# Optimization experiments

Hardware: AMD Instinct MI355X
Metric: run time of the kernel (lower is better)

## Reference

```python
import jax, jax.numpy as jnp
import numpy as np

N, E, C, R, B = 16384, 262144, 256, 9, 4


def _basis_mm(x, coeff, basis):
    # x: [E, Cin], coeff = att[edge_type]: [E, B], basis: [B, Cin, Cout]
    # equals x_e @ (sum_b coeff[e,b] * basis_b) = x_e @ W[edge_type[e]]
    h = jnp.einsum('ec,bco->ebo', x, basis)          # [E, B, Cout]
    return jnp.einsum('ebo,eb->eo', h, coeff)        # [E, Cout]


def _segment_softmax(score, gkey, nseg):
    smax = jax.ops.segment_max(score, gkey, num_segments=nseg)
    ex = jnp.exp(score - smax[gkey])
    den = jax.ops.segment_sum(ex, gkey, num_segments=nseg)
    return ex / den[gkey]


def _attn_branch(rel_emb, basis, att, aw, ab, etypes, seg):
    # relation-specific transform of edge features -> node messages
    m = _basis_mm(rel_emb, att[etypes], basis)                       # [E, Cn]
    # per-relation Linear (weight aw[r], bias ab[r]) + leaky_relu (slope 0.01)
    score = jax.nn.leaky_relu(jnp.sum(m * aw[etypes], -1) + ab[etypes])
    # original: softmax over dest index with -1e8 on edges of other relations,
    # then zeroed by mask == softmax within (dest node, relation) groups
    alpha = _segment_softmax(score, seg * R + etypes, N * R)         # [E]
    agg = jax.ops.segment_sum(alpha[:, None] * m, seg, num_segments=N)  # [N, Cn]
    onehot = jax.nn.one_hot(etypes, R, dtype=m.dtype)
    cnt = jax.ops.segment_sum(onehot, seg, num_segments=N)           # [N, R]
    div = (cnt > 0).astype(m.dtype).sum(-1)
    div = jnp.where(div == 0, jnp.ones_like(div), div)
    return agg / div[:, None]


def setup_inputs():
    key = jax.random.key(0)
    ks = jax.random.split(key, 16)
    p = lambda k, shp: jax.random.normal(k, shp, jnp.float32) * 0.05
    return {
        'edge_index': jax.random.randint(ks[0], (2, E), 0, N, dtype=jnp.int32),
        'nf': jax.random.normal(ks[1], (N, C), jnp.float32),
        'ef': jax.random.normal(ks[2], (E, C), jnp.float32),
        'edge_type_rel': jax.random.randint(ks[3], (E,), 0, R, dtype=jnp.int32),
        'edge_type_rel_inv': jax.random.randint(ks[4], (E,), 0, R, dtype=jnp.int32),
        'edge_norm': jax.random.uniform(ks[5], (E,), jnp.float32),
        'sub2rel_basis': p(ks[6], (B, C, C)),
        'sub2rel_att': p(ks[7], (R, B)),
        'obj2rel_basis': p(ks[8], (B, C, C)),
        'obj2rel_att': p(ks[9], (R, B)),
        'rel2sub_basis': p(ks[10], (B, C, C)),
        'rel2sub_att': p(ks[11], (R, B)),
        'rel2sub_attn_w': p(ks[12], (R, C)),
        'rel2sub_attn_b': jnp.zeros((R,), jnp.float32),
        'rel2obj_basis': p(ks[13], (B, C, C)),
        'rel2obj_att': p(ks[14], (R, B)),
        'rel2obj_attn_w': p(ks[15], (R, C)),
        'rel2obj_attn_b': jnp.zeros((R,), jnp.float32),
    }


def reference(edge_index, nf, ef, edge_type_rel, edge_type_rel_inv, edge_norm,
              sub2rel_basis, sub2rel_att, obj2rel_basis, obj2rel_att,
              rel2sub_basis, rel2sub_att, rel2sub_attn_w, rel2sub_attn_b,
              rel2obj_basis, rel2obj_att, rel2obj_attn_w, rel2obj_attn_b):
    src, dst = edge_index[0], edge_index[1]
    # sub2rel / obj2rel: per-edge relation-specific GEMM (mask+sum over rel in
    # the original collapses to a gather of W by edge type)
    s2r = _basis_mm(nf[src], sub2rel_att[edge_type_rel], sub2rel_basis)
    o2r = _basis_mm(nf[dst], obj2rel_att[edge_type_rel_inv], obj2rel_basis)
    rel_emb = ef + 0.5 * (s2r + o2r)
    # rel2sub aggregates at src (edgeindex_i = edge_index[0], rel types = inv)
    sub_agg = _attn_branch(rel_emb, rel2sub_basis, rel2sub_att,
                           rel2sub_attn_w, rel2sub_attn_b, edge_type_rel_inv, src)
    # rel2obj aggregates at dst (edgeindex_i = edge_index[1], rel types = fwd)
    obj_agg = _attn_branch(rel_emb, rel2obj_basis, rel2obj_att,
                           rel2obj_attn_w, rel2obj_attn_b, edge_type_rel, dst)
    node_emb = nf + 0.5 * (sub_agg + obj_agg)
    return node_emb, rel_emb
```

## Files before the change

### kernel.cpp

```cpp
#include <hip/hip_runtime.h>

#define N_ 16384
#define E_ 262144
#define C_ 256
#define R_ 9
#define B_ 4
#define NKEY (N_ * R_)
#define NKEY2 (2 * NKEY)

typedef unsigned short u16;
typedef unsigned int u32;

typedef __bf16 bf16x8 __attribute__((ext_vector_type(8)));
typedef float f32x4 __attribute__((ext_vector_type(4)));
typedef unsigned short u16x8 __attribute__((ext_vector_type(8)));

__device__ __forceinline__ u16 f2bf(float x) {
  u32 u = __float_as_uint(x);
  u32 r = (u + 0x7fffu + ((u >> 16) & 1u)) >> 16;
  return (u16)r;
}
__device__ __forceinline__ float bf2f(u16 h) {
  return __uint_as_float(((u32)h) << 16);
}

__device__ __forceinline__ void gld16(const void* g, void* l) {
  __builtin_amdgcn_global_load_lds(
      (const __attribute__((address_space(1))) void*)g,
      (__attribute__((address_space(3))) void*)l, 16, 0, 0);
}

__global__ __launch_bounds__(256) void prep_kernel(
    const float* __restrict__ b1, const float* __restrict__ a1,
    const float* __restrict__ b2, const float* __restrict__ a2,
    const float* __restrict__ b3, const float* __restrict__ a3,
    const float* __restrict__ aw3,
    const float* __restrict__ b4, const float* __restrict__ a4,
    const float* __restrict__ aw4,
    u16* __restrict__ W1, u16* __restrict__ W2,
    u16* __restrict__ W3, u16* __restrict__ W4,
    float* __restrict__ v3, float* __restrict__ v4) {
  int c = blockIdx.x, r = blockIdx.y, o = threadIdx.x;
  float s1 = 0.f, s2 = 0.f, s3 = 0.f, s4 = 0.f;
#pragma unroll
  for (int b = 0; b < B_; ++b) {
    long bi = ((long)b * C_ + c) * C_ + o;
    s1 += a1[r * B_ + b] * b1[bi];
    s2 += a2[r * B_ + b] * b2[bi];
    s3 += a3[r * B_ + b] * b3[bi];
    s4 += a4[r * B_ + b] * b4[bi];
  }
  W1[((long)r * C_ + o) * C_ + c] = f2bf(s1);
  W2[((long)r * C_ + o) * C_ + c] = f2bf(s2);
  W3[(long)o * (R_ * C_) + r * C_ + c] = f2bf(s3);
  W4[(long)o * (R_ * C_) + r * C_ + c] = f2bf(s4);

  __shared__ float red[256];
  red[o] = s3 * aw3[r * C_ + o];
  __syncthreads();
  for (int s = 128; s > 0; s >>= 1) {
    if (o < s) red[o] += red[o + s];
    __syncthreads();
  }
  float rv3 = red[0];
  __syncthreads();
  red[o] = s4 * aw4[r * C_ + o];
  __syncthreads();
  for (int s = 128; s > 0; s >>= 1) {
    if (o < s) red[o] += red[o + s];
    __syncthreads();
  }
  if (o == 0) {
    v3[r * C_ + c] = rv3;
    v4[r * C_ + c] = red[0];
  }
}

__global__ void cvt_bf16_kernel(const float* __restrict__ in, u16* __restrict__ out) {
  long i = ((long)blockIdx.x * 256 + threadIdx.x) * 4;
  float4 f = *(const float4*)(in + i);
  ushort4 h;
  h.x = f2bf(f.x); h.y = f2bf(f.y); h.z = f2bf(f.z); h.w = f2bf(f.w);
  *(ushort4*)(out + i) = h;
}

#define BM 128
#define BN 128
#define BK 32

__global__ __launch_bounds__(256) void gemmY_kernel(
    const u16* __restrict__ A, int lda,
    const u16* __restrict__ Bt0, const u16* __restrict__ Bt1, long bBatch, int K,
    u16* __restrict__ Out0, u16* __restrict__ Out1, long cBatch, int ldc) {
  __shared__ __attribute__((aligned(16))) u16 As[BM * BK];
  __shared__ __attribute__((aligned(16))) u16 Bs[BN * BK];

  const int t = threadIdx.x;
  const int m0 = blockIdx.x * BM;
  const int n0 = blockIdx.y * BN;
  const int zb = blockIdx.z;
  const long z = (zb < R_) ? zb : zb - R_;
  const u16* Bt = (zb < R_) ? Bt0 : Bt1;
  u16* Out = (zb < R_) ? Out0 : Out1;

  const int sr = t >> 2;
  const int sk = (t & 3) * 8;

  const int w = t >> 6, lane = t & 63;
  const int wm = (w >> 1) * 64, wn = (w & 1) * 64;
  const int lr = lane & 15;
  const int lk = (lane >> 4) * 8;

  f32x4 acc[4][4];
#pragma unroll
  for (int i = 0; i < 4; ++i)
#pragma unroll
    for (int j = 0; j < 4; ++j) acc[i][j] = (f32x4){0.f, 0.f, 0.f, 0.f};

  const u16* aR = A + (long)(m0 + sr) * lda + sk;
  const u16* bR = Bt + z * bBatch + (long)(n0 + sr) * K + sk;
  const long aStep = 64L * lda;
  const long bStep = 64L * K;

  u16* aD0 = &As[t * 8];
  u16* aD1 = &As[2048 + t * 8];
  u16* bD0 = &Bs[t * 8];
  u16* bD1 = &Bs[2048 + t * 8];

  for (int k0 = 0; k0 < K; k0 += BK) {
    gld16(aR, aD0);
    gld16(aR + aStep, aD1);
    gld16(bR, bD0);
    gld16(bR + bStep, bD1);
    aR += BK;
    bR += BK;
    __syncthreads();

    bf16x8 af[4], bg[4];
#pragma unroll
    for (int mi = 0; mi < 4; ++mi)
      af[mi] = *(const bf16x8*)&As[(wm + mi * 16 + lr) * BK + lk];
#pragma unroll
    for (int ni = 0; ni < 4; ++ni)
      bg[ni] = *(const bf16x8*)&Bs[(wn + ni * 16 + lr) * BK + lk];
#pragma unroll
    for (int mi = 0; mi < 4; ++mi)
#pragma unroll
      for (int ni = 0; ni < 4; ++ni)
        acc[mi][ni] = __builtin_amdgcn_mfma_f32_16x16x32_bf16(af[mi], bg[ni], acc[mi][ni], 0, 0, 0);

    __syncthreads();
  }

  long base = z * cBatch;
#pragma unroll
  for (int mi = 0; mi < 4; ++mi) {
    int rowb = m0 + wm + mi * 16 + ((lane >> 4) * 4);
#pragma unroll
    for (int ni = 0; ni < 4; ++ni) {
      int col = n0 + wn + ni * 16 + lr;
      f32x4 c = acc[mi][ni];
#pragma unroll
      for (int i = 0; i < 4; ++i) {
        long idx = base + (long)(rowb + i) * ldc + col;
        Out[idx] = f2bf(c[i]);
      }
    }
  }
}

__global__ __launch_bounds__(256) void gemmAgg_kernel(
    const u16* __restrict__ AS, const u16* __restrict__ AO,
    const u16* __restrict__ BtS, const u16* __restrict__ BtO,
    float* __restrict__ Out,
    const float* __restrict__ nf,
    const float* __restrict__ divS, const float* __restrict__ divO) {
  const int K = R_ * C_;
  __shared__ __attribute__((aligned(16))) u16 As[64 * BK];
  __shared__ __attribute__((aligned(16))) u16 Bs[BN * BK];

  const int t = threadIdx.x;
  const int m0 = blockIdx.x * 64;
  const int n0 = blockIdx.y * BN;

  const int sr = t >> 2;
  const int sk = (t & 3) * 8;

  const int w = t >> 6, lane = t & 63;
  const int wm = (w >> 1) * 32, wn = (w & 1) * 64;
  const int lr = lane & 15;
  const int lk = (lane >> 4) * 8;

  u16* aD = &As[t * 8];
  u16* bD0 = &Bs[t * 8];
  u16* bD1 = &Bs[2048 + t * 8];
  const long bStep = 64L * K;

  f32x4 accS[2][4], accO[2][4];
#pragma unroll
  for (int i = 0; i < 2; ++i)
#pragma unroll
    for (int j = 0; j < 4; ++j) {
      accS[i][j] = (f32x4){0.f, 0.f, 0.f, 0.f};
      accO[i][j] = (f32x4){0.f, 0.f, 0.f, 0.f};
    }

  {
    const u16* aR = AS + (long)(m0 + sr) * K + sk;
    const u16* bR = BtS + (long)(n0 + sr) * K + sk;
    for (int k0 = 0; k0 < K; k0 += BK) {
      gld16(aR, aD);
      gld16(bR, bD0);
      gld16(bR + bStep, bD1);
      aR += BK;
      bR += BK;
      __syncthreads();
      bf16x8 af[2], bg[4];
#pragma unroll
      for (int mi = 0; mi < 2; ++mi)
        af[mi] = *(const bf16x8*)&As[(wm + mi * 16 + lr) * BK + lk];
#pragma unroll
      for (int ni = 0; ni < 4; ++ni)
        bg[ni] = *(const bf16x8*)&Bs[(wn + ni * 16 + lr) * BK + lk];
#pragma unroll
      for (int mi = 0; mi < 2; ++mi)
#pragma unroll
        for (int ni = 0; ni < 4; ++ni)
          accS[mi][ni] = __builtin_amdgcn_mfma_f32_16x16x32_bf16(af[mi], bg[ni], accS[mi][ni], 0, 0, 0);
      __syncthreads();
    }
  }
  {
    const u16* aR = AO + (long)(m0 + sr) * K + sk;
    const u16* bR = BtO + (long)(n0 + sr) * K + sk;
    for (int k0 = 0; k0 < K; k0 += BK) {
      gld16(aR, aD);
      gld16(bR, bD0);
      gld16(bR + bStep, bD1);
      aR += BK;
      bR += BK;
      __syncthreads();
      bf16x8 af[2], bg[4];
#pragma unroll
      for (int mi = 0; mi < 2; ++mi)
        af[mi] = *(const bf16x8*)&As[(wm + mi * 16 + lr) * BK + lk];
#pragma unroll
      for (int ni = 0; ni < 4; ++ni)
        bg[ni] = *(const bf16x8*)&Bs[(wn + ni * 16 + lr) * BK + lk];
#pragma unroll
      for (int mi = 0; mi < 2; ++mi)
#pragma unroll
        for (int ni = 0; ni < 4; ++ni)
          accO[mi][ni] = __builtin_amdgcn_mfma_f32_16x16x32_bf16(af[mi], bg[ni], accO[mi][ni], 0, 0, 0);
      __syncthreads();
    }
  }

#pragma unroll
  for (int mi = 0; mi < 2; ++mi) {
    int rowb = m0 + wm + mi * 16 + ((lane >> 4) * 4);
    float fsS[4], fsO[4];
#pragma unroll
    for (int i = 0; i < 4; ++i) {
      fsS[i] = 0.5f * divS[rowb + i];
      fsO[i] = 0.5f * divO[rowb + i];
    }
#pragma unroll
    for (int ni = 0; ni < 4; ++ni) {
      int col = n0 + wn + ni * 16 + lr;
      f32x4 cS = accS[mi][ni];
      f32x4 cO = accO[mi][ni];
#pragma unroll
      for (int i = 0; i < 4; ++i) {
        long idx = (long)(rowb + i) * C_ + col;
        Out[idx] = nf[idx] + fsS[i] * cS[i] + fsO[i] * cO[i];
      }
    }
  }
}

__global__ __launch_bounds__(256) void relemb_kernel(
    const float* __restrict__ ef, const u16* __restrict__ Ysub,
    const u16* __restrict__ Yobj, const int* __restrict__ src,
    const int* __restrict__ dst, const int* __restrict__ et,
    const int* __restrict__ eti, const float* __restrict__ vS,
    const float* __restrict__ abS, const float* __restrict__ vO,
    const float* __restrict__ abO, float* __restrict__ rel,
    float* __restrict__ scoreS, float* __restrict__ scoreO,
    int* __restrict__ cnt) {
  int g = threadIdx.x >> 5;
  int h = threadIdx.x & 31;
  int c = h * 8;
  int e0 = blockIdx.x * 16 + g * 2;
  int e1 = e0 + 1;

  int sn0 = src[e0], dn0 = dst[e0], tf0 = et[e0], ti0 = eti[e0];
  int sn1 = src[e1], dn1 = dst[e1], tf1 = et[e1], ti1 = eti[e1];

  u16x8 ys0 = *(const u16x8*)(Ysub + ((long)tf0 * N_ + sn0) * C_ + c);
  u16x8 yo0 = *(const u16x8*)(Yobj + ((long)ti0 * N_ + dn0) * C_ + c);
  u16x8 ys1 = *(const u16x8*)(Ysub + ((long)tf1 * N_ + sn1) * C_ + c);
  u16x8 yo1 = *(const u16x8*)(Yobj + ((long)ti1 * N_ + dn1) * C_ + c);

  long ei0 = (long)e0 * C_ + c;
  long ei1 = (long)e1 * C_ + c;
  f32x4 f00 = *(const f32x4*)(ef + ei0);
  f32x4 f01 = *(const f32x4*)(ef + ei0 + 4);
  f32x4 f10 = *(const f32x4*)(ef + ei1);
  f32x4 f11 = *(const f32x4*)(ef + ei1 + 4);

  float a0 = f00[0] + 0.5f * (bf2f(ys0[0]) + bf2f(yo0[0]));
  float a1 = f00[1] + 0.5f * (bf2f(ys0[1]) + bf2f(yo0[1]));
  float a2 = f00[2] + 0.5f * (bf2f(ys0[2]) + bf2f(yo0[2]));
  float a3 = f00[3] + 0.5f * (bf2f(ys0[3]) + bf2f(yo0[3]));
  float a4 = f01[0] + 0.5f * (bf2f(ys0[4]) + bf2f(yo0[4]));
  float a5 = f01[1] + 0.5f * (bf2f(ys0[5]) + bf2f(yo0[5]));
  float a6 = f01[2] + 0.5f * (bf2f(ys0[6]) + bf2f(yo0[6]));
  float a7 = f01[3] + 0.5f * (bf2f(ys0[7]) + bf2f(yo0[7]));
  *(f32x4*)(rel + ei0) = (f32x4){a0, a1, a2, a3};
  *(f32x4*)(rel + ei0 + 4) = (f32x4){a4, a5, a6, a7};

  float b0 = f10[0] + 0.5f * (bf2f(ys1[0]) + bf2f(yo1[0]));
  float b1 = f10[1] + 0.5f * (bf2f(ys1[1]) + bf2f(yo1[1]));
  float b2 = f10[2] + 0.5f * (bf2f(ys1[2]) + bf2f(yo1[2]));
  float b3 = f10[3] + 0.5f * (bf2f(ys1[3]) + bf2f(yo1[3]));
  float b4 = f11[0] + 0.5f * (bf2f(ys1[4]) + bf2f(yo1[4]));
  float b5 = f11[1] + 0.5f * (bf2f(ys1[5]) + bf2f(yo1[5]));
  float b6 = f11[2] + 0.5f * (bf2f(ys1[6]) + bf2f(yo1[6]));
  float b7 = f11[3] + 0.5f * (bf2f(ys1[7]) + bf2f(yo1[7]));
  *(f32x4*)(rel + ei1) = (f32x4){b0, b1, b2, b3};
  *(f32x4*)(rel + ei1 + 4) = (f32x4){b4, b5, b6, b7};

  float4 w0, w1;
  w0 = *(const float4*)(vS + ti0 * C_ + c);
  w1 = *(const float4*)(vS + ti0 * C_ + c + 4);
  float pS0 = a0 * w0.x + a1 * w0.y + a2 * w0.z + a3 * w0.w +
              a4 * w1.x + a5 * w1.y + a6 * w1.z + a7 * w1.w;
  w0 = *(const float4*)(vO + tf0 * C_ + c);
  w1 = *(const float4*)(vO + tf0 * C_ + c + 4);
  float pO0 = a0 * w0.x + a1 * w0.y + a2 * w0.z + a3 * w0.w +
              a4 * w1.x + a5 * w1.y + a6 * w1.z + a7 * w1.w;
  w0 = *(const float4*)(vS + ti1 * C_ + c);
  w1 = *(const float4*)(vS + ti1 * C_ + c + 4);
  float pS1 = b0 * w0.x + b1 * w0.y + b2 * w0.z + b3 * w0.w +
              b4 * w1.x + b5 * w1.y + b6 * w1.z + b7 * w1.w;
  w0 = *(const float4*)(vO + tf1 * C_ + c);
  w1 = *(const float4*)(vO + tf1 * C_ + c + 4);
  float pO1 = b0 * w0.x + b1 * w0.y + b2 * w0.z + b3 * w0.w +
              b4 * w1.x + b5 * w1.y + b6 * w1.z + b7 * w1.w;

#pragma unroll
  for (int off = 16; off > 0; off >>= 1) {
    pS0 += __shfl_xor(pS0, off);
    pO0 += __shfl_xor(pO0, off);
    pS1 += __shfl_xor(pS1, off);
    pO1 += __shfl_xor(pO1, off);
  }
  if (h == 0) {
    float sS = pS0 + abS[ti0];
    sS = sS > 0.f ? sS : 0.01f * sS;
    scoreS[e0] = sS;
    atomicAdd(&cnt[sn0 * R_ + ti0], 1);
    float sO = pO0 + abO[tf0];
    sO = sO > 0.f ? sO : 0.01f * sO;
    scoreO[e0] = sO;
    atomicAdd(&cnt[NKEY + dn0 * R_ + tf0], 1);

    sS = pS1 + abS[ti1];
    sS = sS > 0.f ? sS : 0.01f * sS;
    scoreS[e1] = sS;
    atomicAdd(&cnt[sn1 * R_ + ti1], 1);
    sO = pO1 + abO[tf1];
    sO = sO > 0.f ? sO : 0.01f * sO;
    scoreO[e1] = sO;
    atomicAdd(&cnt[NKEY + dn1 * R_ + tf1], 1);
  }
}

__global__ __launch_bounds__(256) void div_kernel(const int* __restrict__ cnt,
                                                  float* __restrict__ divS,
                                                  float* __restrict__ divO) {
  int n = blockIdx.x * 256 + threadIdx.x;
  int ds = 0, dq = 0;
#pragma unroll
  for (int r = 0; r < R_; ++r) {
    ds += (cnt[n * R_ + r] > 0);
    dq += (cnt[NKEY + n * R_ + r] > 0);
  }
  divS[n] = ds ? 1.f / (float)ds : 1.f;
  divO[n] = dq ? 1.f / (float)dq : 1.f;
}

__global__ __launch_bounds__(256) void scan1_kernel(const int* __restrict__ cnt,
                                                    int* __restrict__ offs,
                                                    int* __restrict__ part) {
  __shared__ int lds[256];
  int b = blockIdx.x, t = threadIdx.x;
  int base = b * 1024 + t * 4;
  int4 v = *(const int4*)(cnt + base);
  int tsum = v.x + v.y + v.z + v.w;
  lds[t] = tsum;
  __syncthreads();
  for (int d = 1; d < 256; d <<= 1) {
    int x = (t >= d) ? lds[t - d] : 0;
    __syncthreads();
    lds[t] += x;
    __syncthreads();
  }
  int run = (t == 0) ? 0 : lds[t - 1];
  int4 o;
  o.x = run;
  o.y = run + v.x;
  o.z = o.y + v.y;
  o.w = o.z + v.z;
  *(int4*)(offs + base) = o;
  if (t == 255) part[b] = lds[255];
}

__global__ __launch_bounds__(512) void scan2_kernel(int* __restrict__ part) {
  __shared__ int lds[512];
  int t = threadIdx.x;
  lds[t] = (t < 288) ? part[t] : 0;
  __syncthreads();
  for (int d = 1; d < 512; d <<= 1) {
    int x = (t >= d) ? lds[t - d] : 0;
    __syncthreads();
    lds[t] += x;
    __syncthreads();
  }
  if (t < 288) part[t] = (t == 0) ? 0 : lds[t - 1];
}

__global__ __launch_bounds__(256) void scan3_kernel(const int* __restrict__ part,
                                                    int* __restrict__ offs,
                                                    int* __restrict__ cursor) {
  int i = blockIdx.x * 256 + threadIdx.x;
  int v = offs[i] + part[i >> 10];
  offs[i] = v;
  cursor[i] = v;
}

__global__ __launch_bounds__(256) void scatter_kernel(
    const int* __restrict__ et, const int* __restrict__ eti,
    const int* __restrict__ src, const int* __restrict__ dst,
    int* __restrict__ cursor, int* __restrict__ order) {
  int e = blockIdx.x * 256 + threadIdx.x;
  int kS = src[e] * R_ + eti[e];
  int kO = NKEY + dst[e] * R_ + et[e];
  order[atomicAdd(&cursor[kS], 1)] = e;
  order[atomicAdd(&cursor[kO], 1)] = e;
}

__device__ __forceinline__ void zkey_process(
    const float* __restrict__ rel, const float* __restrict__ score,
    const int* __restrict__ order, int len, int sta, int eL, float scL,
    int lane, int c, u16* __restrict__ z, int k2) {
  float ax = 0.f, ay = 0.f, az = 0.f, aw = 0.f;
  if (len == 1) {
    int e = __shfl(eL, 0);
    float4 x = *(const float4*)(rel + (long)e * C_ + c);
    ax = x.x; ay = x.y; az = x.z; aw = x.w;
  } else if (len > 1 && len <= 64) {
    float ex = (lane < len) ? __expf(scL) : 0.f;
    float den = ex;
#pragma unroll
    for (int off = 32; off > 0; off >>= 1) den += __shfl_xor(den, off);
    float inv = 1.f / den;
    int i = 0;
    for (; i + 2 <= len; i += 2) {
      int e0 = __shfl(eL, i);
      int e1 = __shfl(eL, i + 1);
      float a0 = __shfl(ex, i) * inv;
      float a1 = __shfl(ex, i + 1) * inv;
      float4 x0 = *(const float4*)(rel + (long)e0 * C_ + c);
      float4 x1 = *(const float4*)(rel + (long)e1 * C_ + c);
      ax += a0 * x0.x + a1 * x1.x;
      ay += a0 * x0.y + a1 * x1.y;
      az += a0 * x0.z + a1 * x1.z;
      aw += a0 * x0.w + a1 * x1.w;
    }
    if (i < len) {
      int e0 = __shfl(eL, i);
      float a0 = __shfl(ex, i) * inv;
      float4 x0 = *(const float4*)(rel + (long)e0 * C_ + c);
      ax += a0 * x0.x;
      ay += a0 * x0.y;
      az += a0 * x0.z;
      aw += a0 * x0.w;
    }
  } else if (len > 64) {
    float den = 0.f;
    for (int i = 0; i < len; ++i) {
      int e = order[sta + i];
      float ex2 = __expf(score[e]);
      den += ex2;
      float4 x = *(const float4*)(rel + (long)e * C_ + c);
      ax += ex2 * x.x; ay += ex2 * x.y; az += ex2 * x.z; aw += ex2 * x.w;
    }
    float inv = 1.f / den;
    ax *= inv; ay *= inv; az *= inv; aw *= inv;
  }
  int n = k2 / R_, r = k2 - n * R_;
  ushort4 hv;
  hv.x = f2bf(ax); hv.y = f2bf(ay); hv.z = f2bf(az); hv.w = f2bf(aw);
  *(ushort4*)(z + (long)n * (R_ * C_) + r * C_ + c) = hv;
}

__global__ __launch_bounds__(256) void zgather_kernel(
    const float* __restrict__ rel, const float* __restrict__ scoreS,
    const float* __restrict__ scoreO, const int* __restrict__ order,
    const int* __restrict__ offs, const int* __restrict__ cnt,
    u16* __restrict__ zS, u16* __restrict__ zO) {
  int wid = threadIdx.x >> 6;
  int lane = threadIdx.x & 63;
  int c = lane * 4;
  int key0 = (blockIdx.x * 4 + wid) * 4;
  const float* score = scoreS;
  u16* z = zS;
  int kb = key0;
  if (key0 >= NKEY) { score = scoreO; z = zO; kb = key0 - NKEY; }

  int len0 = cnt[key0], len1 = cnt[key0 + 1], len2 = cnt[key0 + 2], len3 = cnt[key0 + 3];
  int sta0 = offs[key0], sta1 = offs[key0 + 1], sta2 = offs[key0 + 2], sta3 = offs[key0 + 3];

  int e0 = 0, e1 = 0, e2 = 0, e3 = 0;
  if (len0 <= 64 && lane < len0) e0 = order[sta0 + lane];
  if (len1 <= 64 && lane < len1) e1 = order[sta1 + lane];
  if (len2 <= 64 && lane < len2) e2 = order[sta2 + lane];
  if (len3 <= 64 && lane < len3) e3 = order[sta3 + lane];

  float s0 = 0.f, s1 = 0.f, s2 = 0.f, s3 = 0.f;
  if (len0 > 1 && len0 <= 64 && lane < len0) s0 = score[e0];
  if (len1 > 1 && len1 <= 64 && lane < len1) s1 = score[e1];
  if (len2 > 1 && len2 <= 64 && lane < len2) s2 = score[e2];
  if (len3 > 1 && len3 <= 64 && lane < len3) s3 = score[e3];

  zkey_process(rel, score, order, len0, sta0, e0, s0, lane, c, z, kb + 0);
  zkey_process(rel, score, order, len1, sta1, e1, s1, lane, c, z, kb + 1);
  zkey_process(rel, score, order, len2, sta2, e2, s2, lane, c, z, kb + 2);
  zkey_process(rel, score, order, len3, sta3, e3, s3, lane, c, z, kb + 3);
}

extern "C" void kernel_launch(void* const* d_in, const int* in_sizes, int n_in,
                              void* d_out, int out_size, void* d_ws, size_t ws_size,
                              hipStream_t stream) {
  const int* edge_index = (const int*)d_in[0];
  const float* nf = (const float*)d_in[1];
  const float* ef = (const float*)d_in[2];
  const int* et = (const int*)d_in[3];
  const int* eti = (const int*)d_in[4];
  const float* s2r_basis = (const float*)d_in[6];
  const float* s2r_att = (const float*)d_in[7];
  const float* o2r_basis = (const float*)d_in[8];
  const float* o2r_att = (const float*)d_in[9];
  const float* r2s_basis = (const float*)d_in[10];
  const float* r2s_att = (const float*)d_in[11];
  const float* r2s_aw = (const float*)d_in[12];
  const float* r2s_ab = (const float*)d_in[13];
  const float* r2o_basis = (const float*)d_in[14];
  const float* r2o_att = (const float*)d_in[15];
  const float* r2o_aw = (const float*)d_in[16];
  const float* r2o_ab = (const float*)d_in[17];

  const int* src = edge_index;
  const int* dst = edge_index + E_;

  char* ws = (char*)d_ws;
  u16* WtSub = (u16*)(ws + 0);
  u16* WtObj = (u16*)(ws + 1179648);
  u16* WtR2S = (u16*)(ws + 2359296);
  u16* WtR2O = (u16*)(ws + 3538944);
  float* vS = (float*)(ws + 4718592);
  float* vO = (float*)(ws + 4727808);
  u16* nfb = (u16*)(ws + 4737024);
  float* scoreS = (float*)(ws + 13125632);
  float* scoreO = (float*)(ws + 14174208);
  int* cnt = (int*)(ws + 15222784);
  int* offs = (int*)(ws + 16402432);
  int* cursor = (int*)(ws + 17582080);
  int* order = (int*)(ws + 18761728);
  int* part = (int*)(ws + 20858880);
  float* divS = (float*)(ws + 20860928);
  float* divO = (float*)(ws + 20926464);
  u16* Ysub = (u16*)(ws + 20992000);
  u16* Yobj = (u16*)(ws + 96489472);
  u16* zS = Ysub;
  u16* zO = Yobj;

  float* node_out = (float*)d_out;
  float* rel_out = (float*)d_out + (long)N_ * C_;

  prep_kernel<<<dim3(C_, R_), 256, 0, stream>>>(
      s2r_basis, s2r_att, o2r_basis, o2r_att,
      r2s_basis, r2s_att, r2s_aw, r2o_basis, r2o_att, r2o_aw,
      WtSub, WtObj, WtR2S, WtR2O, vS, vO);
  cvt_bf16_kernel<<<(N_ * C_) / 1024, 256, 0, stream>>>(nf, nfb);
  (void)hipMemsetAsync(cnt, 0, (size_t)NKEY2 * 4, stream);

  gemmY_kernel<<<dim3(N_ / BM, C_ / BN, 2 * R_), 256, 0, stream>>>(
      nfb, C_, WtSub, WtObj, (long)C_ * C_, C_, Ysub, Yobj, (long)N_ * C_, C_);

  relemb_kernel<<<E_ / 16, 256, 0, stream>>>(ef, Ysub, Yobj, src, dst, et, eti,
                                             vS, r2s_ab, vO, r2o_ab, rel_out,
                                             scoreS, scoreO, cnt);
  div_kernel<<<N_ / 256, 256, 0, stream>>>(cnt, divS, divO);

  scan1_kernel<<<288, 256, 0, stream>>>(cnt, offs, part);
  scan2_kernel<<<1, 512, 0, stream>>>(part);
  scan3_kernel<<<NKEY2 / 256, 256, 0, stream>>>(part, offs, cursor);
  scatter_kernel<<<E_ / 256, 256, 0, stream>>>(et, eti, src, dst, cursor, order);
  zgather_kernel<<<NKEY2 / 16, 256, 0, stream>>>(rel_out, scoreS, scoreO, order,
                                                 offs, cnt, zS, zO);

  gemmAgg_kernel<<<dim3(N_ / 64, C_ / BN), 256, 0, stream>>>(
      zS, zO, WtR2S, WtR2O, node_out, nf, divS, divO);

  (void)in_sizes; (void)n_in; (void)out_size; (void)ws_size;
}
```

Baseline: 908.0 us.

## Write bf16 copy of rel_emb for gather, swap gemmAgg grid order

relemb_kernel now also writes a bf16 copy of each edge's relation embedding, and uses one 64-lane wave per edge with 4 channels per lane. zgather reads this bf16 copy instead of the fp32 output, which halves the bytes moved by its random-access gather. The len==1 path copies the bf16 value directly without a round trip through float. gemmAgg's grid is transposed so that blocks sharing the same rows run next to each other, which should improve L2 reuse of the A operand. The cost is an extra 128MB write and slightly lower precision in the aggregated messages.

```diff
diff --git a/kernel.cpp b/kernel.cpp
--- a/kernel.cpp
+++ b/kernel.cpp
@@ -13,7 +13,6 @@
 
 typedef __bf16 bf16x8 __attribute__((ext_vector_type(8)));
 typedef float f32x4 __attribute__((ext_vector_type(4)));
-typedef unsigned short u16x8 __attribute__((ext_vector_type(8)));
 
 __device__ __forceinline__ u16 f2bf(float x) {
   u32 u = __float_as_uint(x);
@@ -180,8 +179,8 @@
   __shared__ __attribute__((aligned(16))) u16 Bs[BN * BK];
 
   const int t = threadIdx.x;
-  const int m0 = blockIdx.x * 64;
-  const int n0 = blockIdx.y * BN;
+  const int m0 = blockIdx.y * 64;
+  const int n0 = blockIdx.x * BN;
 
   const int sr = t >> 2;
   const int sk = (t & 3) * 8;
@@ -286,77 +285,63 @@
     const int* __restrict__ eti, const float* __restrict__ vS,
     const float* __restrict__ abS, const float* __restrict__ vO,
     const float* __restrict__ abO, float* __restrict__ rel,
+    u16* __restrict__ relB,
     float* __restrict__ scoreS, float* __restrict__ scoreO,
     int* __restrict__ cnt) {
-  int g = threadIdx.x >> 5;
-  int h = threadIdx.x & 31;
-  int c = h * 8;
-  int e0 = blockIdx.x * 16 + g * 2;
+  int wv = threadIdx.x >> 6;
+  int lane = threadIdx.x & 63;
+  int c = lane * 4;
+  int e0 = blockIdx.x * 8 + wv * 2;
   int e1 = e0 + 1;
 
   int sn0 = src[e0], dn0 = dst[e0], tf0 = et[e0], ti0 = eti[e0];
   int sn1 = src[e1], dn1 = dst[e1], tf1 = et[e1], ti1 = eti[e1];
 
-  u16x8 ys0 = *(const u16x8*)(Ysub + ((long)tf0 * N_ + sn0) * C_ + c);
-  u16x8 yo0 = *(const u16x8*)(Yobj + ((long)ti0 * N_ + dn0) * C_ + c);
-  u16x8 ys1 = *(const u16x8*)(Ysub + ((long)tf1 * N_ + sn1) * C_ + c);
-  u16x8 yo1 = *(const u16x8*)(Yobj + ((long)ti1 * N_ + dn1) * C_ + c);
+  ushort4 ys0 = *(const ushort4*)(Ysub + ((long)tf0 * N_ + sn0) * C_ + c);
+  ushort4 yo0 = *(const ushort4*)(Yobj + ((long)ti0 * N_ + dn0) * C_ + c);
+  ushort4 ys1 = *(const ushort4*)(Ysub + ((long)tf1 * N_ + sn1) * C_ + c);
+  ushort4 yo1 = *(const ushort4*)(Yobj + ((long)ti1 * N_ + dn1) * C_ + c);
 
   long ei0 = (long)e0 * C_ + c;
   long ei1 = (long)e1 * C_ + c;
-  f32x4 f00 = *(const f32x4*)(ef + ei0);
-  f32x4 f01 = *(const f32x4*)(ef + ei0 + 4);
-  f32x4 f10 = *(const f32x4*)(ef + ei1);
-  f32x4 f11 = *(const f32x4*)(ef + ei1 + 4);
-
-  float a0 = f00[0] + 0.5f * (bf2f(ys0[0]) + bf2f(yo0[0]));
-  float a1 = f00[1] + 0.5f * (bf2f(ys0[1]) + bf2f(yo0[1]));
-  float a2 = f00[2] + 0.5f * (bf2f(ys0[2]) + bf2f(yo0[2]));
-  float a3 = f00[3] + 0.5f * (bf2f(ys0[3]) + bf2f(yo0[3]));
-  float a4 = f01[0] + 0.5f * (bf2f(ys0[4]) + bf2f(yo0[4]));
-  float a5 = f01[1] + 0.5f * (bf2f(ys0[5]) + bf2f(yo0[5]));
-  float a6 = f01[2] + 0.5f * (bf2f(ys0[6]) + bf2f(yo0[6]));
-  float a7 = f01[3] + 0.5f * (bf2f(ys0[7]) + bf2f(yo0[7]));
-  *(f32x4*)(rel + ei0) = (f32x4){a0, a1, a2, a3};
-  *(f32x4*)(rel + ei0 + 4) = (f32x4){a4, a5, a6, a7};
-
-  float b0 = f10[0] + 0.5f * (bf2f(ys1[0]) + bf2f(yo1[0]));
-  float b1 = f10[1] + 0.5f * (bf2f(ys1[1]) + bf2f(yo1[1]));
-  float b2 = f10[2] + 0.5f * (bf2f(ys1[2]) + bf2f(yo1[2]));
-  float b3 = f10[3] + 0.5f * (bf2f(ys1[3]) + bf2f(yo1[3]));
-  float b4 = f11[0] + 0.5f * (bf2f(ys1[4]) + bf2f(yo1[4]));
-  float b5 = f11[1] + 0.5f * (bf2f(ys1[5]) + bf2f(yo1[5]));
-  float b6 = f11[2] + 0.5f * (bf2f(ys1[6]) + bf2f(yo1[6]));
-  float b7 = f11[3] + 0.5f * (bf2f(ys1[7]) + bf2f(yo1[7]));
-  *(f32x4*)(rel + ei1) = (f32x4){b0, b1, b2, b3};
-  *(f32x4*)(rel + ei1 + 4) = (f32x4){b4, b5, b6, b7};
-
-  float4 w0, w1;
-  w0 = *(const float4*)(vS + ti0 * C_ + c);
-  w1 = *(const float4*)(vS + ti0 * C_ + c + 4);
-  float pS0 = a0 * w0.x + a1 * w0.y + a2 * w0.z + a3 * w0.w +
-              a4 * w1.x + a5 * w1.y + a6 * w1.z + a7 * w1.w;
-  w0 = *(const float4*)(vO + tf0 * C_ + c);
-  w1 = *(const float4*)(vO + tf0 * C_ + c + 4);
-  float pO0 = a0 * w0.x + a1 * w0.y + a2 * w0.z + a3 * w0.w +
-              a4 * w1.x + a5 * w1.y + a6 * w1.z + a7 * w1.w;
-  w0 = *(const float4*)(vS + ti1 * C_ + c);
-  w1 = *(const float4*)(vS + ti1 * C_ + c + 4);
-  float pS1 = b0 * w0.x + b1 * w0.y + b2 * w0.z + b3 * w0.w +
-              b4 * w1.x + b5 * w1.y + b6 * w1.z + b7 * w1.w;
-  w0 = *(const float4*)(vO + tf1 * C_ + c);
-  w1 = *(const float4*)(vO + tf1 * C_ + c + 4);
-  float pO1 = b0 * w0.x + b1 * w0.y + b2 * w0.z + b3 * w0.w +
-              b4 * w1.x + b5 * w1.y + b6 * w1.z + b7 * w1.w;
-
-#pragma unroll
-  for (int off = 16; off > 0; off >>= 1) {
+  float4 f0 = *(const float4*)(ef + ei0);
+  float4 f1 = *(const float4*)(ef + ei1);
+
+  float a0 = f0.x + 0.5f * (bf2f(ys0.x) + bf2f(yo0.x));
+  float a1 = f0.y + 0.5f * (bf2f(ys0.y) + bf2f(yo0.y));
+  float a2 = f0.z + 0.5f * (bf2f(ys0.z) + bf2f(yo0.z));
+  float a3 = f0.w + 0.5f * (bf2f(ys0.w) + bf2f(yo0.w));
+  float b0 = f1.x + 0.5f * (bf2f(ys1.x) + bf2f(yo1.x));
+  float b1 = f1.y + 0.5f * (bf2f(ys1.y) + bf2f(yo1.y));
+  float b2 = f1.z + 0.5f * (bf2f(ys1.z) + bf2f(yo1.z));
+  float b3 = f1.w + 0.5f * (bf2f(ys1.w) + bf2f(yo1.w));
+
+  *(float4*)(rel + ei0) = (float4){a0, a1, a2, a3};
+  *(float4*)(rel + ei1) = (float4){b0, b1, b2, b3};
+  ushort4 h0, h1;
+  h0.x = f2bf(a0); h0.y = f2bf(a1); h0.z = f2bf(a2); h0.w = f2bf(a3);
+  h1.x = f2bf(b0); h1.y = f2bf(b1); h1.z = f2bf(b2); h1.w = f2bf(b3);
+  *(ushort4*)(relB + ei0) = h0;
+  *(ushort4*)(relB + ei1) = h1;
+
+  float4 w;
+  w = *(const float4*)(vS + ti0 * C_ + c);
+  float pS0 = a0 * w.x + a1 * w.y + a2 * w.z + a3 * w.w;
+  w = *(const float4*)(vO + tf0 * C_ + c);
+  float pO0 = a0 * w.x + a1 * w.y + a2 * w.z + a3 * w.w;
+  w = *(const float4*)(vS + ti1 * C_ + c);
+  float pS1 = b0 * w.x + b1 * w.y + b2 * w.z + b3 * w.w;
+  w = *(const float4*)(vO + tf1 * C_ + c);
+  float pO1 = b0 * w.x + b1 * w.y + b2 * w.z + b3 * w.w;
+
+#pragma unroll
+  for (int off = 32; off > 0; off >>= 1) {
     pS0 += __shfl_xor(pS0, off);
     pO0 += __shfl_xor(pO0, off);
     pS1 += __shfl_xor(pS1, off);
     pO1 += __shfl_xor(pO1, off);
   }
-  if (h == 0) {
+  if (lane == 0) {
     float sS = pS0 + abS[ti0];
     sS = sS > 0.f ? sS : 0.01f * sS;
     scoreS[e0] = sS;
@@ -452,62 +437,64 @@
 }
 
 __device__ __forceinline__ void zkey_process(
-    const float* __restrict__ rel, const float* __restrict__ score,
+    const u16* __restrict__ relB, const float* __restrict__ score,
     const int* __restrict__ order, int len, int sta, int eL, float scL,
     int lane, int c, u16* __restrict__ z, int k2) {
   float ax = 0.f, ay = 0.f, az = 0.f, aw = 0.f;
+  ushort4 hv;
   if (len == 1) {
     int e = __shfl(eL, 0);
-    float4 x = *(const float4*)(rel + (long)e * C_ + c);
-    ax = x.x; ay = x.y; az = x.z; aw = x.w;
-  } else if (len > 1 && len <= 64) {
-    float ex = (lane < len) ? __expf(scL) : 0.f;
-    float den = ex;
-#pragma unroll
-    for (int off = 32; off > 0; off >>= 1) den += __shfl_xor(den, off);
-    float inv = 1.f / den;
-    int i = 0;
-    for (; i + 2 <= len; i += 2) {
-      int e0 = __shfl(eL, i);
-      int e1 = __shfl(eL, i + 1);
-      float a0 = __shfl(ex, i) * inv;
-      float a1 = __shfl(ex, i + 1) * inv;
-      float4 x0 = *(const float4*)(rel + (long)e0 * C_ + c);
-      float4 x1 = *(const float4*)(rel + (long)e1 * C_ + c);
-      ax += a0 * x0.x + a1 * x1.x;
-      ay += a0 * x0.y + a1 * x1.y;
-      az += a0 * x0.z + a1 * x1.z;
-      aw += a0 * x0.w + a1 * x1.w;
+    hv = *(const ushort4*)(relB + (long)e * C_ + c);
+  } else {
+    if (len > 1 && len <= 64) {
+      float ex = (lane < len) ? __expf(scL) : 0.f;
+      float den = ex;
+#pragma unroll
+      for (int off = 32; off > 0; off >>= 1) den += __shfl_xor(den, off);
+      float inv = 1.f / den;
+      int i = 0;
+      for (; i + 2 <= len; i += 2) {
+        int e0 = __shfl(eL, i);
+        int e1 = __shfl(eL, i + 1);
+        float a0 = __shfl(ex, i) * inv;
+        float a1 = __shfl(ex, i + 1) * inv;
+        ushort4 x0 = *(const ushort4*)(relB + (long)e0 * C_ + c);
+        ushort4 x1 = *(const ushort4*)(relB + (long)e1 * C_ + c);
+        ax += a0 * bf2f(x0.x) + a1 * bf2f(x1.x);
+        ay += a0 * bf2f(x0.y) + a1 * bf2f(x1.y);
+        az += a0 * bf2f(x0.z) + a1 * bf2f(x1.z);
+        aw += a0 * bf2f(x0.w) + a1 * bf2f(x1.w);
+      }
+      if (i < len) {
+        int e0 = __shfl(eL, i);
+        float a0 = __shfl(ex, i) * inv;
+        ushort4 x0 = *(const ushort4*)(relB + (long)e0 * C_ + c);
+        ax += a0 * bf2f(x0.x);
+        ay += a0 * bf2f(x0.y);
+        az += a0 * bf2f(x0.z);
+        aw += a0 * bf2f(x0.w);
+      }
+    } else if (len > 64) {
+      float den = 0.f;
+      for (int i = 0; i < len; ++i) {
+        int e = order[sta + i];
+        float ex2 = __expf(score[e]);
+        den += ex2;
+        ushort4 x = *(const ushort4*)(relB + (long)e * C_ + c);
+        ax += ex2 * bf2f(x.x); ay += ex2 * bf2f(x.y);
+        az += ex2 * bf2f(x.z); aw += ex2 * bf2f(x.w);
+      }
+      float inv = 1.f / den;
+      ax *= inv; ay *= inv; az *= inv; aw *= inv;
     }
-    if (i < len) {
-      int e0 = __shfl(eL, i);
-      float a0 = __shfl(ex, i) * inv;
-      float4 x0 = *(const float4*)(rel + (long)e0 * C_ + c);
-      ax += a0 * x0.x;
-      ay += a0 * x0.y;
-      az += a0 * x0.z;
-      aw += a0 * x0.w;
-    }
-  } else if (len > 64) {
-    float den = 0.f;
-    for (int i = 0; i < len; ++i) {
-      int e = order[sta + i];
-      float ex2 = __expf(score[e]);
-      den += ex2;
-      float4 x = *(const float4*)(rel + (long)e * C_ + c);
-      ax += ex2 * x.x; ay += ex2 * x.y; az += ex2 * x.z; aw += ex2 * x.w;
-    }
-    float inv = 1.f / den;
-    ax *= inv; ay *= inv; az *= inv; aw *= inv;
+    hv.x = f2bf(ax); hv.y = f2bf(ay); hv.z = f2bf(az); hv.w = f2bf(aw);
   }
   int n = k2 / R_, r = k2 - n * R_;
-  ushort4 hv;
-  hv.x = f2bf(ax); hv.y = f2bf(ay); hv.z = f2bf(az); hv.w = f2bf(aw);
   *(ushort4*)(z + (long)n * (R_ * C_) + r * C_ + c) = hv;
 }
 
 __global__ __launch_bounds__(256) void zgather_kernel(
-    const float* __restrict__ rel, const float* __restrict__ scoreS,
+    const u16* __restrict__ relB, const float* __restrict__ scoreS,
     const float* __restrict__ scoreO, const int* __restrict__ order,
     const int* __restrict__ offs, const int* __restrict__ cnt,
     u16* __restrict__ zS, u16* __restrict__ zO) {
@@ -535,10 +522,10 @@
   if (len2 > 1 && len2 <= 64 && lane < len2) s2 = score[e2];
   if (len3 > 1 && len3 <= 64 && lane < len3) s3 = score[e3];
 
-  zkey_process(rel, score, order, len0, sta0, e0, s0, lane, c, z, kb + 0);
-  zkey_process(rel, score, order, len1, sta1, e1, s1, lane, c, z, kb + 1);
-  zkey_process(rel, score, order, len2, sta2, e2, s2, lane, c, z, kb + 2);
-  zkey_process(rel, score, order, len3, sta3, e3, s3, lane, c, z, kb + 3);
+  zkey_process(relB, score, order, len0, sta0, e0, s0, lane, c, z, kb + 0);
+  zkey_process(relB, score, order, len1, sta1, e1, s1, lane, c, z, kb + 1);
+  zkey_process(relB, score, order, len2, sta2, e2, s2, lane, c, z, kb + 2);
+  zkey_process(relB, score, order, len3, sta3, e3, s3, lane, c, z, kb + 3);
 }
 
 extern "C" void kernel_launch(void* const* d_in, const int* in_sizes, int n_in,
@@ -584,6 +571,7 @@
   float* divO = (float*)(ws + 20926464);
   u16* Ysub = (u16*)(ws + 20992000);
   u16* Yobj = (u16*)(ws + 96489472);
+  u16* relB = (u16*)(ws + 171986944);
   u16* zS = Ysub;
   u16* zO = Yobj;
 
@@ -600,19 +588,19 @@
   gemmY_kernel<<<dim3(N_ / BM, C_ / BN, 2 * R_), 256, 0, stream>>>(
       nfb, C_, WtSub, WtObj, (long)C_ * C_, C_, Ysub, Yobj, (long)N_ * C_, C_);
 
-  relemb_kernel<<<E_ / 16, 256, 0, stream>>>(ef, Ysub, Yobj, src, dst, et, eti,
-                                             vS, r2s_ab, vO, r2o_ab, rel_out,
-                                             scoreS, scoreO, cnt);
+  relemb_kernel<<<E_ / 8, 256, 0, stream>>>(ef, Ysub, Yobj, src, dst, et, eti,
+                                            vS, r2s_ab, vO, r2o_ab, rel_out,
+                                            relB, scoreS, scoreO, cnt);
   div_kernel<<<N_ / 256, 256, 0, stream>>>(cnt, divS, divO);
 
   scan1_kernel<<<288, 256, 0, stream>>>(cnt, offs, part);
   scan2_kernel<<<1, 512, 0, stream>>>(part);
   scan3_kernel<<<NKEY2 / 256, 256, 0, stream>>>(part, offs, cursor);
   scatter_kernel<<<E_ / 256, 256, 0, stream>>>(et, eti, src, dst, cursor, order);
-  zgather_kernel<<<NKEY2 / 16, 256, 0, stream>>>(rel_out, scoreS, scoreO, order,
+  zgather_kernel<<<NKEY2 / 16, 256, 0, stream>>>(relB, scoreS, scoreO, order,
                                                  offs, cnt, zS, zO);
 
-  gemmAgg_kernel<<<dim3(N_ / 64, C_ / BN), 256, 0, stream>>>(
+  gemmAgg_kernel<<<dim3(C_ / BN, N_ / 64), 256, 0, stream>>>(
       zS, zO, WtR2S, WtR2O, node_out, nf, divS, divO);
 
   (void)in_sizes; (void)n_in; (void)out_size; (void)ws_size;
```

Measured after the change: 879.0 us. 3.2% less time.
